# Performance work log

Hardware: AMD Instinct MI355X
Metric: run time of the kernel (lower is better)

Reference implementation:

```python
import jax, jax.numpy as jnp
import numpy as np

LATENT_SIZE = 1024
WORD_SIZE = 64
NB_WORD = 8192
COMMIT_VQ = 2.5
BATCH = 2048


def setup_inputs() -> dict:
    key = jax.random.key(0)
    k1, k2, k3 = jax.random.split(key, 3)
    z_mean = jax.random.normal(k1, (BATCH, LATENT_SIZE), dtype=jnp.float32)
    z_log_var = jax.random.normal(k2, (BATCH, LATENT_SIZE), dtype=jnp.float32)
    # Embedding initialized uniform(-1/nb_word, 1/nb_word) in the torch module;
    # use normal here for a numerically non-degenerate correctness baseline.
    emb_weight = jax.random.normal(k3, (NB_WORD, WORD_SIZE), dtype=jnp.float32)
    return {"z_mean": z_mean, "z_log_var": z_log_var, "emb_weight": emb_weight}


def reference(z_mean, z_log_var, emb_weight):
    sg = jax.lax.stop_gradient
    input_shape = z_mean.shape
    # (B * latent/word, word)
    z = z_mean.reshape(-1, LATENT_SIZE // WORD_SIZE, WORD_SIZE)
    z_flat = z.reshape(-1, WORD_SIZE)
    # squared euclidean distances: (N, nb_word)
    distances = (
        jnp.sum(z_flat ** 2, axis=1, keepdims=True)
        + jnp.sum(emb_weight ** 2, axis=1)
        - 2.0 * jnp.einsum("bd,nd->bn", z_flat, emb_weight)
    )
    min_idx = jnp.argmin(distances, axis=1)  # (N,)
    z_q = emb_weight[min_idx].reshape(z.shape)  # gather codebook vectors
    loss = (
        jnp.mean((sg(z_q) - z) ** 2)
        + COMMIT_VQ * jnp.mean((z_q - sg(z)) ** 2)
    )
    z_q_st = z + sg(z_q - z)  # straight-through estimator
    return z_q_st.reshape(input_shape), loss
```

## Files before the change

kernel.cpp:

```cpp
#include <hip/hip_runtime.h>
#include <math.h>

#define LATENT   1024
#define WORD     64
#define NB_WORD  8192
#define BATCH    2048
#define NROWS    (BATCH * LATENT / WORD)
#define NELEM    (BATCH * LATENT)

#define NCHUNK   8
#define CWCHUNK  (NB_WORD / NCHUNK)
#define TPC      (CWCHUNK / 16)
#define NTILE    (NB_WORD / 16)
#define PKTS     (NTILE * 6 * 64)

typedef __attribute__((ext_vector_type(8))) __bf16 bf16x8;
typedef __attribute__((ext_vector_type(4))) float  f32x4;

__global__ __launch_bounds__(256) void vq_prep_kernel(
    const float* __restrict__ emb, float* __restrict__ e2,
    bf16x8* __restrict__ epack) {
    int m = blockIdx.x * 256 + threadIdx.x;
    int tile = m >> 4, l15 = m & 15;
    float s0 = 0.f, s1 = 0.f, s2 = 0.f, s3 = 0.f;
#pragma unroll
    for (int Ks = 0; Ks < 2; ++Ks) {
#pragma unroll
        for (int q = 0; q < 4; ++q) {
            const float4* s4 = reinterpret_cast<const float4*>(
                emb + (size_t)m * WORD + Ks * 32 + q * 8);
            float4 a = s4[0], b = s4[1];
            float tv[8] = {a.x, a.y, a.z, a.w, b.x, b.y, b.z, b.w};
            bf16x8 oh, om, ol;
#pragma unroll
            for (int e = 0; e < 8; ++e) {
                float v = tv[e];
                if ((e & 3) == 0) s0 = fmaf(v, v, s0);
                else if ((e & 3) == 1) s1 = fmaf(v, v, s1);
                else if ((e & 3) == 2) s2 = fmaf(v, v, s2);
                else s3 = fmaf(v, v, s3);
                __bf16 h  = (__bf16)v;
                float r1  = v - (float)h;
                __bf16 mm = (__bf16)r1;
                float r2  = r1 - (float)mm;
                __bf16 lo = (__bf16)r2;
                oh[e] = h; om[e] = mm; ol[e] = lo;
            }
            size_t base = ((size_t)tile * 6) * 64 + q * 16 + l15;
            epack[base + (size_t)(0 * 2 + Ks) * 64] = oh;
            epack[base + (size_t)(1 * 2 + Ks) * 64] = om;
            epack[base + (size_t)(2 * 2 + Ks) * 64] = ol;
        }
    }
    e2[m] = (s0 + s1) + (s2 + s3);
}

__device__ __forceinline__ void gload_lds16(const char* g, char* l) {
    __builtin_amdgcn_global_load_lds(
        (const __attribute__((address_space(1))) void*)g,
        (__attribute__((address_space(3))) void*)l, 16, 0, 0);
}

__global__ __launch_bounds__(256)
__attribute__((amdgpu_waves_per_eu(4, 8)))
void vq_argmin_kernel(
    const float* __restrict__ z, const bf16x8* __restrict__ epack,
    const float* __restrict__ e2, unsigned long long* __restrict__ best) {

    {
        int ph = blockIdx.x & 3;
        if (ph == 1) __builtin_amdgcn_s_sleep(2);
        else if (ph == 2) __builtin_amdgcn_s_sleep(4);
        else if (ph == 3) __builtin_amdgcn_s_sleep(6);
    }

    __shared__ __align__(16) char le[2 * 6144];

    const int tid   = threadIdx.x;
    const int lane  = tid & 63;
    const int wband = tid >> 6;
    const int l15   = lane & 15;
    const int l4    = lane >> 4;
    const int rowbase   = blockIdx.x * 128 + wband * 32;
    const int tile0     = blockIdx.y * TPC;
    const int chunkbase = blockIdx.y * CWCHUNK;
    const float* e2g    = e2 + chunkbase;
    const int off       = (blockIdx.x & 15) * 4;

    bf16x8 A[2][2][3];
    const float4* zf4 = reinterpret_cast<const float4*>(z);
#pragma unroll
    for (int mt = 0; mt < 2; ++mt) {
        int row = rowbase + mt * 16 + l15;
#pragma unroll
        for (int Ks = 0; Ks < 2; ++Ks) {
            float4 v0 = zf4[(size_t)row * 16 + Ks * 8 + l4 * 2];
            float4 v1 = zf4[(size_t)row * 16 + Ks * 8 + l4 * 2 + 1];
            float tv[8] = {v0.x, v0.y, v0.z, v0.w, v1.x, v1.y, v1.z, v1.w};
#pragma unroll
            for (int e = 0; e < 8; ++e) {
                float v = tv[e];
                __bf16 h  = (__bf16)v;
                float r1  = v - (float)h;
                __bf16 m  = (__bf16)r1;
                float r2  = r1 - (float)m;
                __bf16 lo = (__bf16)r2;
                A[mt][Ks][0][e] = h;
                A[mt][Ks][1][e] = m;
                A[mt][Ks][2][e] = lo;
            }
        }
    }

    {
        const char* src = (const char*)epack + (size_t)(tile0 + off) * 6144;
        gload_lds16(src + wband * 1024 + lane * 16, le + wband * 1024);
        if (wband < 2)
            gload_lds16(src + (4 + wband) * 1024 + lane * 16,
                        le + (4 + wband) * 1024);
    }
    float e2next = e2g[off * 16 + l15];

    float bestd[8] = {INFINITY, INFINITY, INFINITY, INFINITY,
                      INFINITY, INFINITY, INFINITY, INFINITY};
    int   bt[8]    = {0, 0, 0, 0, 0, 0, 0, 0};

    f32x4 pacc0 = {0.f, 0.f, 0.f, 0.f};
    f32x4 pacc1 = {0.f, 0.f, 0.f, 0.f};
    float e2prev = INFINITY;
    int   tprev  = 0;

    for (int tt = 0; tt < TPC; ++tt) {
        const int buf = tt & 1;
        const int t   = (tt + off) & (TPC - 1);

        asm volatile("s_waitcnt vmcnt(0)" ::: "memory");
        __builtin_amdgcn_sched_barrier(0);
        __builtin_amdgcn_s_barrier();

        const float e2v = e2next;

        {
            const int tn = (tt + 1 + off) & (TPC - 1);
            const char* src = (const char*)epack + (size_t)(tile0 + tn) * 6144;
            char* dst = le + (buf ^ 1) * 6144;
            gload_lds16(src + wband * 1024 + lane * 16, dst + wband * 1024);
            if (wband < 2)
                gload_lds16(src + (4 + wband) * 1024 + lane * 16,
                            dst + (4 + wband) * 1024);
            e2next = e2g[tn * 16 + l15];
        }

        const char* b0 = le + buf * 6144 + lane * 16;
        bf16x8 Bh0 = *reinterpret_cast<const bf16x8*>(b0);
        bf16x8 Bm0 = *reinterpret_cast<const bf16x8*>(b0 + 2048);
        bf16x8 Bl0 = *reinterpret_cast<const bf16x8*>(b0 + 4096);
        bf16x8 Bh1 = *reinterpret_cast<const bf16x8*>(b0 + 1024);
        bf16x8 Bm1 = *reinterpret_cast<const bf16x8*>(b0 + 3072);
        bf16x8 Bl1 = *reinterpret_cast<const bf16x8*>(b0 + 5120);

#pragma unroll
        for (int v = 0; v < 4; ++v) {
            float d0 = fmaf(-2.0f, pacc0[v], e2prev);
            if (d0 < bestd[v])     { bestd[v]     = d0; bt[v]     = tprev; }
            float d1 = fmaf(-2.0f, pacc1[v], e2prev);
            if (d1 < bestd[4 + v]) { bestd[4 + v] = d1; bt[4 + v] = tprev; }
        }

        f32x4 acc0 = {0.f, 0.f, 0.f, 0.f};
        f32x4 acc1 = {0.f, 0.f, 0.f, 0.f};
        __builtin_amdgcn_s_setprio(1);
        acc0 = __builtin_amdgcn_mfma_f32_16x16x32_bf16(A[0][0][0], Bh0, acc0, 0, 0, 0);
        acc1 = __builtin_amdgcn_mfma_f32_16x16x32_bf16(A[1][0][0], Bh0, acc1, 0, 0, 0);
        acc0 = __builtin_amdgcn_mfma_f32_16x16x32_bf16(A[0][0][1], Bh0, acc0, 0, 0, 0);
        acc1 = __builtin_amdgcn_mfma_f32_16x16x32_bf16(A[1][0][1], Bh0, acc1, 0, 0, 0);
        acc0 = __builtin_amdgcn_mfma_f32_16x16x32_bf16(A[0][0][2], Bh0, acc0, 0, 0, 0);
        acc1 = __builtin_amdgcn_mfma_f32_16x16x32_bf16(A[1][0][2], Bh0, acc1, 0, 0, 0);
        acc0 = __builtin_amdgcn_mfma_f32_16x16x32_bf16(A[0][0][0], Bm0, acc0, 0, 0, 0);
        acc1 = __builtin_amdgcn_mfma_f32_16x16x32_bf16(A[1][0][0], Bm0, acc1, 0, 0, 0);
        acc0 = __builtin_amdgcn_mfma_f32_16x16x32_bf16(A[0][0][1], Bm0, acc0, 0, 0, 0);
        acc1 = __builtin_amdgcn_mfma_f32_16x16x32_bf16(A[1][0][1], Bm0, acc1, 0, 0, 0);
        acc0 = __builtin_amdgcn_mfma_f32_16x16x32_bf16(A[0][0][0], Bl0, acc0, 0, 0, 0);
        acc1 = __builtin_amdgcn_mfma_f32_16x16x32_bf16(A[1][0][0], Bl0, acc1, 0, 0, 0);
        acc0 = __builtin_amdgcn_mfma_f32_16x16x32_bf16(A[0][1][0], Bh1, acc0, 0, 0, 0);
        acc1 = __builtin_amdgcn_mfma_f32_16x16x32_bf16(A[1][1][0], Bh1, acc1, 0, 0, 0);
        acc0 = __builtin_amdgcn_mfma_f32_16x16x32_bf16(A[0][1][1], Bh1, acc0, 0, 0, 0);
        acc1 = __builtin_amdgcn_mfma_f32_16x16x32_bf16(A[1][1][1], Bh1, acc1, 0, 0, 0);
        acc0 = __builtin_amdgcn_mfma_f32_16x16x32_bf16(A[0][1][2], Bh1, acc0, 0, 0, 0);
        acc1 = __builtin_amdgcn_mfma_f32_16x16x32_bf16(A[1][1][2], Bh1, acc1, 0, 0, 0);
        acc0 = __builtin_amdgcn_mfma_f32_16x16x32_bf16(A[0][1][0], Bm1, acc0, 0, 0, 0);
        acc1 = __builtin_amdgcn_mfma_f32_16x16x32_bf16(A[1][1][0], Bm1, acc1, 0, 0, 0);
        acc0 = __builtin_amdgcn_mfma_f32_16x16x32_bf16(A[0][1][1], Bm1, acc0, 0, 0, 0);
        acc1 = __builtin_amdgcn_mfma_f32_16x16x32_bf16(A[1][1][1], Bm1, acc1, 0, 0, 0);
        acc0 = __builtin_amdgcn_mfma_f32_16x16x32_bf16(A[0][1][0], Bl1, acc0, 0, 0, 0);
        acc1 = __builtin_amdgcn_mfma_f32_16x16x32_bf16(A[1][1][0], Bl1, acc1, 0, 0, 0);
        __builtin_amdgcn_s_setprio(0);

        pacc0 = acc0; pacc1 = acc1; e2prev = e2v; tprev = t;
    }

#pragma unroll
    for (int v = 0; v < 4; ++v) {
        float d0 = fmaf(-2.0f, pacc0[v], e2prev);
        if (d0 < bestd[v])     { bestd[v]     = d0; bt[v]     = tprev; }
        float d1 = fmaf(-2.0f, pacc1[v], e2prev);
        if (d1 < bestd[4 + v]) { bestd[4 + v] = d1; bt[4 + v] = tprev; }
    }

#pragma unroll
    for (int mt = 0; mt < 2; ++mt) {
#pragma unroll
        for (int v = 0; v < 4; ++v) {
            float bd = bestd[mt * 4 + v];
            int   cw = chunkbase + bt[mt * 4 + v] * 16 + l15;
            unsigned db = __float_as_uint(bd);
            db = (db & 0x80000000u) ? ~db : (db | 0x80000000u);
            unsigned long long key =
                ((unsigned long long)db << 32) | (unsigned)cw;
#pragma unroll
            for (int off2 = 1; off2 < 16; off2 <<= 1) {
                unsigned long long o = __shfl_xor(key, off2);
                key = (o < key) ? o : key;
            }
            if (l15 == 0)
                atomicMin(&best[rowbase + mt * 16 + l4 * 4 + v], key);
        }
    }
}

__global__ __launch_bounds__(256) void vq_out_kernel(
    const float* __restrict__ z, const float* __restrict__ emb,
    const unsigned long long* __restrict__ best,
    float* __restrict__ out, float* __restrict__ lsum) {
    const int base = (blockIdx.x * 256 + threadIdx.x) * 8;
    const int row  = base >> 6;
    const int m    = (int)(best[row] & 0xFFFFFFFFull);

    const float4* zp = reinterpret_cast<const float4*>(z + base);
    const float4* qp = reinterpret_cast<const float4*>(emb + (size_t)m * WORD + (base & 63));
    float4* op = reinterpret_cast<float4*>(out + base);

    float s = 0.f;
#pragma unroll
    for (int i = 0; i < 2; ++i) {
        float4 zv = zp[i];
        float4 qv = qp[i];
        float dx = qv.x - zv.x, dy = qv.y - zv.y, dz = qv.z - zv.z, dw = qv.w - zv.w;
        float4 ov;
        ov.x = zv.x + dx; ov.y = zv.y + dy; ov.z = zv.z + dz; ov.w = zv.w + dw;
        op[i] = ov;
        s += dx*dx + dy*dy + dz*dz + dw*dw;
    }

#pragma unroll
    for (int off = 32; off > 0; off >>= 1) s += __shfl_down(s, off);
    __shared__ float wsum[4];
    int lane = threadIdx.x & 63, wid = threadIdx.x >> 6;
    if (lane == 0) wsum[wid] = s;
    __syncthreads();
    if (threadIdx.x == 0)
        atomicAdd(lsum, (wsum[0] + wsum[1]) + (wsum[2] + wsum[3]));
}

__global__ void vq_loss_kernel(const float* __restrict__ lsum,
                               float* __restrict__ loss_out) {
    float mean = lsum[0] * (1.0f / (float)NELEM);
    loss_out[0] = mean + 2.5f * mean;
}

extern "C" void kernel_launch(void* const* d_in, const int* in_sizes, int n_in,
                              void* d_out, int out_size, void* d_ws, size_t ws_size,
                              hipStream_t stream) {
    const float* z   = (const float*)d_in[0];
    const float* emb = (const float*)d_in[2];
    float* out = (float*)d_out;

    bf16x8* epack = (bf16x8*)d_ws;
    float*  e2    = (float*)((char*)d_ws + (size_t)PKTS * 16);
    unsigned long long* best =
        (unsigned long long*)((char*)e2 + NB_WORD * sizeof(float));
    float* lsum = (float*)((char*)best + NROWS * sizeof(unsigned long long));

    hipMemsetAsync(best, 0xFF, NROWS * sizeof(unsigned long long), stream);
    hipMemsetAsync(lsum, 0, sizeof(float), stream);

    vq_prep_kernel<<<NB_WORD / 256, 256, 0, stream>>>(emb, e2, epack);
    vq_argmin_kernel<<<dim3(NROWS / 128, NCHUNK), 256, 0, stream>>>(
        z, epack, e2, best);
    vq_out_kernel<<<NELEM / (256 * 8), 256, 0, stream>>>(z, emb, best, out, lsum);
    vq_loss_kernel<<<1, 1, 0, stream>>>(lsum, out + NELEM);
}
```

Baseline: 189.6 us.

## Load codebook tiles directly into registers instead of LDS double buffering

Replaces the LDS double-buffered codebook staging, with its per-tile barriers and staggered start sleeps, with per-wave direct global loads into registers, prefetching the next tile. The argmin update now runs on the current accumulators instead of being deferred one iteration, and some MFMA issue order is shuffled. This removes block-wide synchronization, but each wave now fetches the same tile separately, raising L2/global traffic and exposing load latency.

```diff
diff --git a/kernel.cpp b/kernel.cpp
--- a/kernel.cpp
+++ b/kernel.cpp
@@ -55,26 +55,11 @@
     e2[m] = (s0 + s1) + (s2 + s3);
 }
 
-__device__ __forceinline__ void gload_lds16(const char* g, char* l) {
-    __builtin_amdgcn_global_load_lds(
-        (const __attribute__((address_space(1))) void*)g,
-        (__attribute__((address_space(3))) void*)l, 16, 0, 0);
-}
-
 __global__ __launch_bounds__(256)
 __attribute__((amdgpu_waves_per_eu(4, 8)))
 void vq_argmin_kernel(
     const float* __restrict__ z, const bf16x8* __restrict__ epack,
     const float* __restrict__ e2, unsigned long long* __restrict__ best) {
-
-    {
-        int ph = blockIdx.x & 3;
-        if (ph == 1) __builtin_amdgcn_s_sleep(2);
-        else if (ph == 2) __builtin_amdgcn_s_sleep(4);
-        else if (ph == 3) __builtin_amdgcn_s_sleep(6);
-    }
-
-    __shared__ __align__(16) char le[2 * 6144];
 
     const int tid   = threadIdx.x;
     const int lane  = tid & 63;
@@ -112,60 +97,22 @@
         }
     }
 
-    {
-        const char* src = (const char*)epack + (size_t)(tile0 + off) * 6144;
-        gload_lds16(src + wband * 1024 + lane * 16, le + wband * 1024);
-        if (wband < 2)
-            gload_lds16(src + (4 + wband) * 1024 + lane * 16,
-                        le + (4 + wband) * 1024);
-    }
-    float e2next = e2g[off * 16 + l15];
+    const bf16x8* ep0 = epack + (size_t)(tile0 + off) * 384;
+    bf16x8 Bh0 = ep0[lane];
+    bf16x8 Bh1 = ep0[64  + lane];
+    bf16x8 Bm0 = ep0[128 + lane];
+    bf16x8 Bm1 = ep0[192 + lane];
+    bf16x8 Bl0 = ep0[256 + lane];
+    bf16x8 Bl1 = ep0[320 + lane];
+    float e2v  = e2g[off * 16 + l15];
 
     float bestd[8] = {INFINITY, INFINITY, INFINITY, INFINITY,
                       INFINITY, INFINITY, INFINITY, INFINITY};
     int   bt[8]    = {0, 0, 0, 0, 0, 0, 0, 0};
 
-    f32x4 pacc0 = {0.f, 0.f, 0.f, 0.f};
-    f32x4 pacc1 = {0.f, 0.f, 0.f, 0.f};
-    float e2prev = INFINITY;
-    int   tprev  = 0;
-
     for (int tt = 0; tt < TPC; ++tt) {
-        const int buf = tt & 1;
-        const int t   = (tt + off) & (TPC - 1);
-
-        asm volatile("s_waitcnt vmcnt(0)" ::: "memory");
-        __builtin_amdgcn_sched_barrier(0);
-        __builtin_amdgcn_s_barrier();
-
-        const float e2v = e2next;
-
-        {
-            const int tn = (tt + 1 + off) & (TPC - 1);
-            const char* src = (const char*)epack + (size_t)(tile0 + tn) * 6144;
-            char* dst = le + (buf ^ 1) * 6144;
-            gload_lds16(src + wband * 1024 + lane * 16, dst + wband * 1024);
-            if (wband < 2)
-                gload_lds16(src + (4 + wband) * 1024 + lane * 16,
-                            dst + (4 + wband) * 1024);
-            e2next = e2g[tn * 16 + l15];
-        }
-
-        const char* b0 = le + buf * 6144 + lane * 16;
-        bf16x8 Bh0 = *reinterpret_cast<const bf16x8*>(b0);
-        bf16x8 Bm0 = *reinterpret_cast<const bf16x8*>(b0 + 2048);
-        bf16x8 Bl0 = *reinterpret_cast<const bf16x8*>(b0 + 4096);
-        bf16x8 Bh1 = *reinterpret_cast<const bf16x8*>(b0 + 1024);
-        bf16x8 Bm1 = *reinterpret_cast<const bf16x8*>(b0 + 3072);
-        bf16x8 Bl1 = *reinterpret_cast<const bf16x8*>(b0 + 5120);
-
-#pragma unroll
-        for (int v = 0; v < 4; ++v) {
-            float d0 = fmaf(-2.0f, pacc0[v], e2prev);
-            if (d0 < bestd[v])     { bestd[v]     = d0; bt[v]     = tprev; }
-            float d1 = fmaf(-2.0f, pacc1[v], e2prev);
-            if (d1 < bestd[4 + v]) { bestd[4 + v] = d1; bt[4 + v] = tprev; }
-        }
+        const int t  = (tt + off) & (TPC - 1);
+        const int tn = (tt + 1 + off) & (TPC - 1);
 
         f32x4 acc0 = {0.f, 0.f, 0.f, 0.f};
         f32x4 acc1 = {0.f, 0.f, 0.f, 0.f};
@@ -176,10 +123,10 @@
         acc1 = __builtin_amdgcn_mfma_f32_16x16x32_bf16(A[1][0][1], Bh0, acc1, 0, 0, 0);
         acc0 = __builtin_amdgcn_mfma_f32_16x16x32_bf16(A[0][0][2], Bh0, acc0, 0, 0, 0);
         acc1 = __builtin_amdgcn_mfma_f32_16x16x32_bf16(A[1][0][2], Bh0, acc1, 0, 0, 0);
+        acc0 = __builtin_amdgcn_mfma_f32_16x16x32_bf16(A[0][0][1], Bm0, acc0, 0, 0, 0);
+        acc1 = __builtin_amdgcn_mfma_f32_16x16x32_bf16(A[1][0][1], Bm0, acc1, 0, 0, 0);
         acc0 = __builtin_amdgcn_mfma_f32_16x16x32_bf16(A[0][0][0], Bm0, acc0, 0, 0, 0);
         acc1 = __builtin_amdgcn_mfma_f32_16x16x32_bf16(A[1][0][0], Bm0, acc1, 0, 0, 0);
-        acc0 = __builtin_amdgcn_mfma_f32_16x16x32_bf16(A[0][0][1], Bm0, acc0, 0, 0, 0);
-        acc1 = __builtin_amdgcn_mfma_f32_16x16x32_bf16(A[1][0][1], Bm0, acc1, 0, 0, 0);
         acc0 = __builtin_amdgcn_mfma_f32_16x16x32_bf16(A[0][0][0], Bl0, acc0, 0, 0, 0);
         acc1 = __builtin_amdgcn_mfma_f32_16x16x32_bf16(A[1][0][0], Bl0, acc1, 0, 0, 0);
         acc0 = __builtin_amdgcn_mfma_f32_16x16x32_bf16(A[0][1][0], Bh1, acc0, 0, 0, 0);
@@ -188,23 +135,31 @@
         acc1 = __builtin_amdgcn_mfma_f32_16x16x32_bf16(A[1][1][1], Bh1, acc1, 0, 0, 0);
         acc0 = __builtin_amdgcn_mfma_f32_16x16x32_bf16(A[0][1][2], Bh1, acc0, 0, 0, 0);
         acc1 = __builtin_amdgcn_mfma_f32_16x16x32_bf16(A[1][1][2], Bh1, acc1, 0, 0, 0);
+        acc0 = __builtin_amdgcn_mfma_f32_16x16x32_bf16(A[0][1][1], Bm1, acc0, 0, 0, 0);
+        acc1 = __builtin_amdgcn_mfma_f32_16x16x32_bf16(A[1][1][1], Bm1, acc1, 0, 0, 0);
         acc0 = __builtin_amdgcn_mfma_f32_16x16x32_bf16(A[0][1][0], Bm1, acc0, 0, 0, 0);
         acc1 = __builtin_amdgcn_mfma_f32_16x16x32_bf16(A[1][1][0], Bm1, acc1, 0, 0, 0);
-        acc0 = __builtin_amdgcn_mfma_f32_16x16x32_bf16(A[0][1][1], Bm1, acc0, 0, 0, 0);
-        acc1 = __builtin_amdgcn_mfma_f32_16x16x32_bf16(A[1][1][1], Bm1, acc1, 0, 0, 0);
         acc0 = __builtin_amdgcn_mfma_f32_16x16x32_bf16(A[0][1][0], Bl1, acc0, 0, 0, 0);
         acc1 = __builtin_amdgcn_mfma_f32_16x16x32_bf16(A[1][1][0], Bl1, acc1, 0, 0, 0);
         __builtin_amdgcn_s_setprio(0);
 
-        pacc0 = acc0; pacc1 = acc1; e2prev = e2v; tprev = t;
-    }
-
-#pragma unroll
-    for (int v = 0; v < 4; ++v) {
-        float d0 = fmaf(-2.0f, pacc0[v], e2prev);
-        if (d0 < bestd[v])     { bestd[v]     = d0; bt[v]     = tprev; }
-        float d1 = fmaf(-2.0f, pacc1[v], e2prev);
-        if (d1 < bestd[4 + v]) { bestd[4 + v] = d1; bt[4 + v] = tprev; }
+        const bf16x8* epn = epack + (size_t)(tile0 + tn) * 384;
+        Bh0 = epn[lane];
+        Bh1 = epn[64  + lane];
+        Bm0 = epn[128 + lane];
+        Bm1 = epn[192 + lane];
+        Bl0 = epn[256 + lane];
+        Bl1 = epn[320 + lane];
+        const float e2cur = e2v;
+        e2v = e2g[tn * 16 + l15];
+
+#pragma unroll
+        for (int v = 0; v < 4; ++v) {
+            float d0 = fmaf(-2.0f, acc0[v], e2cur);
+            if (d0 < bestd[v])     { bestd[v]     = d0; bt[v]     = t; }
+            float d1 = fmaf(-2.0f, acc1[v], e2cur);
+            if (d1 < bestd[4 + v]) { bestd[4 + v] = d1; bt[4 + v] = t; }
+        }
     }
 
 #pragma unroll
```

Measured after the change: 196.6 us. +3.7%, slower.

## Fold memsets into prep kernel and loss finalize into out kernel

Applied to the files above, without the earlier changes.

The two hipMemsetAsync calls are removed, and the prep kernel now initializes the best-index buffer, the loss accumulator and a new completion counter. The separate single-thread loss kernel is dropped: the last block of the output kernel, found through an atomic counter with thread fences, computes the final loss. The order of two MFMA pairs in the argmin loop is also swapped. This removes three launches or memset operations per call, in exchange for an atomic counter and fences in the output kernel.

```diff
diff --git a/kernel.cpp b/kernel.cpp
--- a/kernel.cpp
+++ b/kernel.cpp
@@ -14,14 +14,24 @@
 #define NTILE    (NB_WORD / 16)
 #define PKTS     (NTILE * 6 * 64)
 
+#define OUT_GRID (NELEM / (256 * 8))
+
 typedef __attribute__((ext_vector_type(8))) __bf16 bf16x8;
 typedef __attribute__((ext_vector_type(4))) float  f32x4;
 
 __global__ __launch_bounds__(256) void vq_prep_kernel(
     const float* __restrict__ emb, float* __restrict__ e2,
-    bf16x8* __restrict__ epack) {
+    bf16x8* __restrict__ epack, unsigned long long* __restrict__ best,
+    float* __restrict__ lsum, unsigned* __restrict__ counter) {
     int m = blockIdx.x * 256 + threadIdx.x;
     int tile = m >> 4, l15 = m & 15;
+
+    best[m]                = ~0ull;
+    best[m + NB_WORD]      = ~0ull;
+    best[m + 2 * NB_WORD]  = ~0ull;
+    best[m + 3 * NB_WORD]  = ~0ull;
+    if (m == 0) { lsum[0] = 0.f; counter[0] = 0u; }
+
     float s0 = 0.f, s1 = 0.f, s2 = 0.f, s3 = 0.f;
 #pragma unroll
     for (int Ks = 0; Ks < 2; ++Ks) {
@@ -188,10 +198,10 @@
         acc1 = __builtin_amdgcn_mfma_f32_16x16x32_bf16(A[1][1][1], Bh1, acc1, 0, 0, 0);
         acc0 = __builtin_amdgcn_mfma_f32_16x16x32_bf16(A[0][1][2], Bh1, acc0, 0, 0, 0);
         acc1 = __builtin_amdgcn_mfma_f32_16x16x32_bf16(A[1][1][2], Bh1, acc1, 0, 0, 0);
+        acc0 = __builtin_amdgcn_mfma_f32_16x16x32_bf16(A[0][1][1], Bm1, acc0, 0, 0, 0);
+        acc1 = __builtin_amdgcn_mfma_f32_16x16x32_bf16(A[1][1][1], Bm1, acc1, 0, 0, 0);
         acc0 = __builtin_amdgcn_mfma_f32_16x16x32_bf16(A[0][1][0], Bm1, acc0, 0, 0, 0);
         acc1 = __builtin_amdgcn_mfma_f32_16x16x32_bf16(A[1][1][0], Bm1, acc1, 0, 0, 0);
-        acc0 = __builtin_amdgcn_mfma_f32_16x16x32_bf16(A[0][1][1], Bm1, acc0, 0, 0, 0);
-        acc1 = __builtin_amdgcn_mfma_f32_16x16x32_bf16(A[1][1][1], Bm1, acc1, 0, 0, 0);
         acc0 = __builtin_amdgcn_mfma_f32_16x16x32_bf16(A[0][1][0], Bl1, acc0, 0, 0, 0);
         acc1 = __builtin_amdgcn_mfma_f32_16x16x32_bf16(A[1][1][0], Bl1, acc1, 0, 0, 0);
         __builtin_amdgcn_s_setprio(0);
@@ -231,7 +241,8 @@
 __global__ __launch_bounds__(256) void vq_out_kernel(
     const float* __restrict__ z, const float* __restrict__ emb,
     const unsigned long long* __restrict__ best,
-    float* __restrict__ out, float* __restrict__ lsum) {
+    float* __restrict__ out, float* __restrict__ lsum,
+    unsigned* __restrict__ counter) {
     const int base = (blockIdx.x * 256 + threadIdx.x) * 8;
     const int row  = base >> 6;
     const int m    = (int)(best[row] & 0xFFFFFFFFull);
@@ -258,14 +269,18 @@
     int lane = threadIdx.x & 63, wid = threadIdx.x >> 6;
     if (lane == 0) wsum[wid] = s;
     __syncthreads();
-    if (threadIdx.x == 0)
-        atomicAdd(lsum, (wsum[0] + wsum[1]) + (wsum[2] + wsum[3]));
-}
-
-__global__ void vq_loss_kernel(const float* __restrict__ lsum,
-                               float* __restrict__ loss_out) {
-    float mean = lsum[0] * (1.0f / (float)NELEM);
-    loss_out[0] = mean + 2.5f * mean;
+    if (threadIdx.x == 0) {
+        float bsum = (wsum[0] + wsum[1]) + (wsum[2] + wsum[3]);
+        atomicAdd(lsum, bsum);
+        __threadfence();
+        unsigned old = atomicAdd(counter, 1u);
+        if (old == (unsigned)(OUT_GRID - 1)) {
+            __threadfence();
+            float total = atomicAdd(lsum, 0.0f);
+            float mean  = total * (1.0f / (float)NELEM);
+            out[NELEM]  = mean + 2.5f * mean;
+        }
+    }
 }
 
 extern "C" void kernel_launch(void* const* d_in, const int* in_sizes, int n_in,
@@ -279,14 +294,13 @@
     float*  e2    = (float*)((char*)d_ws + (size_t)PKTS * 16);
     unsigned long long* best =
         (unsigned long long*)((char*)e2 + NB_WORD * sizeof(float));
-    float* lsum = (float*)((char*)best + NROWS * sizeof(unsigned long long));
-
-    hipMemsetAsync(best, 0xFF, NROWS * sizeof(unsigned long long), stream);
-    hipMemsetAsync(lsum, 0, sizeof(float), stream);
-
-    vq_prep_kernel<<<NB_WORD / 256, 256, 0, stream>>>(emb, e2, epack);
+    float*    lsum    = (float*)((char*)best + NROWS * sizeof(unsigned long long));
+    unsigned* counter = (unsigned*)(lsum + 1);
+
+    vq_prep_kernel<<<NB_WORD / 256, 256, 0, stream>>>(
+        emb, e2, epack, best, lsum, counter);
     vq_argmin_kernel<<<dim3(NROWS / 128, NCHUNK), 256, 0, stream>>>(
         z, epack, e2, best);
-    vq_out_kernel<<<NELEM / (256 * 8), 256, 0, stream>>>(z, emb, best, out, lsum);
-    vq_loss_kernel<<<1, 1, 0, stream>>>(lsum, out + NELEM);
-}
+    vq_out_kernel<<<OUT_GRID, 256, 0, stream>>>(
+        z, emb, best, out, lsum, counter);
+}
```

Result: slower. 206.3 us (+8.8%).
